# Performance work log

Hardware: AMD Instinct MI355X
Metric: run time of the kernel (lower is better)

The kernel has to match this reference:

```python
import jax, jax.numpy as jnp
import numpy as np

DIM = 768
HEADS = 12
HD = DIM // HEADS
E = 8
R = 64
ALPHA = 128.0
LORA_SCALE = ALPHA / R  # 2.0
ENABLE_BITS = np.array([1.0, 0.0, 1.0], dtype=np.float32)  # LoRA on q and v slices of qkv


def setup_inputs() -> dict:
    key = jax.random.key(0)
    ks = jax.random.split(key, 8)
    x = jax.random.normal(ks[0], (2, 4096, DIM), jnp.float32)
    # base (frozen) weights, shared across experts; no biases (qkv_bias=False)
    Wqkv = jax.random.normal(ks[1], (3 * DIM, DIM), jnp.float32) * 0.02
    Wproj = jax.random.normal(ks[2], (DIM, DIM), jnp.float32) * 0.02
    # per-expert LoRA adapters. qkv: shared down-proj A, per-output-slice up-proj B,
    # masked by enable bits (q,k,v).
    Aqkv = jax.random.normal(ks[3], (E, R, DIM), jnp.float32) * 0.02
    Bqkv = jax.random.normal(ks[4], (E, 3, DIM, R), jnp.float32) * 0.02
    Bqkv = Bqkv * jnp.asarray(ENABLE_BITS)[None, :, None, None]
    Aproj = jax.random.normal(ks[5], (E, R, DIM), jnp.float32) * 0.02
    Bproj = jax.random.normal(ks[6], (E, DIM, R), jnp.float32) * 0.02
    expert_indices = np.arange(4, dtype=np.int64) % E  # static per-chunk routing
    chunk_sizes = np.array([1024, 1024, 1024, 1024], dtype=np.int64)
    return {"x": x, "Wqkv": Wqkv, "Aqkv": Aqkv, "Bqkv": Bqkv, "Wproj": Wproj,
            "Aproj": Aproj, "Bproj": Bproj, "expert_indices": expert_indices,
            "chunk_sizes": chunk_sizes}


def reference(x, Wqkv, Aqkv, Bqkv, Wproj, Aproj, Bproj, expert_indices, chunk_sizes):
    # chunk sizes / expert indices are static host-side routing metadata
    sizes = [int(c) for c in np.asarray(chunk_sizes)]
    eidx = [int(e) for e in np.asarray(expert_indices)]
    offs = np.concatenate([[0], np.cumsum(sizes)])
    B = x.shape[0]
    scale = HD ** -0.5
    last_k = None
    last_v = None
    outs = []
    for i, n in enumerate(sizes):
        xc = x[:, offs[i]:offs[i + 1]]            # [B, n, DIM]
        e = eidx[i]
        # LoRA-adapted qkv for this chunk's expert
        base = xc @ Wqkv.T                        # [B, n, 3*DIM]
        h = xc @ Aqkv[e].T                        # [B, n, R]
        delta = jnp.einsum('bnr,tdr->bntd', h, Bqkv[e]).reshape(B, n, 3 * DIM)
        qkv = (base + LORA_SCALE * delta).reshape(B, n, 3, HEADS, HD)
        qkv = qkv.transpose(2, 0, 3, 1, 4)        # [3, B, H, n, HD]
        q, k, v = qkv[0], qkv[1], qkv[2]
        if last_k is not None:                    # growing KV over chunks (chunk-causal)
            k = jnp.concatenate([last_k, k], axis=-2)
            v = jnp.concatenate([last_v, v], axis=-2)
        last_k, last_v = k, v
        attn = jax.nn.softmax(jnp.einsum('bhqd,bhkd->bhqk', q * scale, k), axis=-1)
        o = jnp.einsum('bhqk,bhkd->bhqd', attn, v)
        o = o.transpose(0, 2, 1, 3).reshape(B, n, DIM)
        # LoRA-adapted output projection for the same expert
        o = o @ Wproj.T + LORA_SCALE * ((o @ Aproj[e].T) @ Bproj[e].T)
        outs.append(o)
    return jnp.concatenate(outs, axis=1)          # [B, total, DIM]
```

## Files before the change

kernel.cpp:

```cpp
#include <hip/hip_runtime.h>
#include <math.h>

#define BATCH   2
#define SEQ     4096
#define DIMD    768
#define NHEADS  12
#define HDIM    64
#define RR      64
#define CHUNK   1024
#define NTOK    (BATCH * SEQ)
#define BHN     (BATCH * NHEADS)
#define PITCH   88
#define KC2     2304
#define QSCALE  0.18033688011112042f

typedef __attribute__((ext_vector_type(8))) short short8;
typedef __attribute__((ext_vector_type(4))) float f32x4;

#define AS1 __attribute__((address_space(1)))
#define AS3 __attribute__((address_space(3)))

__device__ __forceinline__ void glds16(const void* g, void* l) {
    __builtin_amdgcn_global_load_lds((const AS1 unsigned int*)g,
                                     (AS3 unsigned int*)l, 16, 0, 0);
}

__device__ __forceinline__ float dot4(const float4 a, const float4 b) {
    float s = a.x * b.x;
    s = fmaf(a.y, b.y, s);
    s = fmaf(a.z, b.z, s);
    s = fmaf(a.w, b.w, s);
    return s;
}

__device__ __forceinline__ unsigned short f2bf(float x) {
    union { float f; unsigned u; } c; c.f = x;
    unsigned u = c.u + 0x7fffu + ((c.u >> 16) & 1u);
    return (unsigned short)(u >> 16);
}
__device__ __forceinline__ float bf2f(unsigned short h) {
    union { unsigned u; float f; } c; c.u = ((unsigned)h) << 16;
    return c.f;
}
__device__ __forceinline__ unsigned pack2bf(float a, float b) {
    union { float f; unsigned u; } x, y; x.f = a; y.f = b;
    unsigned ua = x.u + 0x7fffu + ((x.u >> 16) & 1u);
    unsigned ub = y.u + 0x7fffu + ((y.u >> 16) & 1u);
    return (ua >> 16) | (ub & 0xffff0000u);
}

__global__ __launch_bounds__(256)
void combine_split(const float* __restrict__ W, const float* __restrict__ A,
                   const float* __restrict__ Bm, int NB,
                   unsigned short* __restrict__ out)
{
    const int tid = threadIdx.x;
    const int ty = tid >> 4, tx = tid & 15;
    const int f0 = blockIdx.x * 64, d0 = blockIdx.y * 64, e = blockIdx.z;

    __shared__ float Bb[64][68];
    __shared__ float Aa[64][68];

    const float* Ae = A + (long)e * RR * DIMD;
    const float* Be = Bm + (long)e * NB * RR;

    const int lrow = tid >> 2, lc = (tid & 3) * 16;
    #pragma unroll
    for (int u = 0; u < 16; u += 4)
        *(float4*)&Bb[lrow][lc + u] = *(const float4*)&Be[(long)(f0 + lrow) * RR + lc + u];
    #pragma unroll
    for (int u = 0; u < 16; u++)
        Aa[lc + u][lrow] = Ae[(long)lrow * DIMD + d0 + lc + u];
    __syncthreads();

    float acc[4][4] = {};
    #pragma unroll
    for (int r4 = 0; r4 < RR; r4 += 4) {
        float4 a[4], b[4];
        #pragma unroll
        for (int i = 0; i < 4; i++) a[i] = *(float4*)&Bb[ty + 16 * i][r4];
        #pragma unroll
        for (int j = 0; j < 4; j++) b[j] = *(float4*)&Aa[tx + 16 * j][r4];
        #pragma unroll
        for (int i = 0; i < 4; i++)
            #pragma unroll
            for (int j = 0; j < 4; j++)
                acc[i][j] += dot4(a[i], b[j]);
    }

    #pragma unroll
    for (int i = 0; i < 4; i++) {
        const int f = f0 + ty + 16 * i;
        unsigned short* o = out + ((long)e * NB + f) * KC2;
        #pragma unroll
        for (int j = 0; j < 4; j++) {
            const int d = d0 + tx + 16 * j;
            const float val = W[(long)f * DIMD + d] + 2.0f * acc[i][j];
            const unsigned short hi = f2bf(val);
            const unsigned short lo = f2bf(val - bf2f(hi));
            o[d] = hi; o[768 + d] = lo; o[1536 + d] = hi;
        }
    }
}

__global__ __launch_bounds__(192)
void build_xa2(const float* __restrict__ X, unsigned short* __restrict__ out)
{
    const int tok = blockIdx.x;
    const int j = threadIdx.x * 4;
    const float* xr = X + (long)tok * DIMD;
    unsigned short* o = out + (long)tok * KC2;
    float4 v = *(const float4*)&xr[j];
    unsigned short h0 = f2bf(v.x), h1 = f2bf(v.y), h2 = f2bf(v.z), h3 = f2bf(v.w);
    unsigned short l0 = f2bf(v.x - bf2f(h0)), l1 = f2bf(v.y - bf2f(h1));
    unsigned short l2 = f2bf(v.z - bf2f(h2)), l3 = f2bf(v.w - bf2f(h3));
    uint2 hp, lp;
    hp.x = (unsigned)h0 | ((unsigned)h1 << 16);
    hp.y = (unsigned)h2 | ((unsigned)h3 << 16);
    lp.x = (unsigned)l0 | ((unsigned)l1 << 16);
    lp.y = (unsigned)l2 | ((unsigned)l3 << 16);
    *(uint2*)&o[j] = hp;
    *(uint2*)&o[768 + j] = hp;
    *(uint2*)&o[1536 + j] = lp;
}

template<int MODE>
__global__ __launch_bounds__(256)
void mfma_gemm(const unsigned short* __restrict__ A,
               const unsigned short* __restrict__ B, int NB, int n_base,
               unsigned short* __restrict__ qpl, unsigned short* __restrict__ kpl,
               unsigned short* __restrict__ vpl, float* __restrict__ outf)
{
    __shared__ __align__(16) unsigned short lA[128 * 64];
    __shared__ __align__(16) unsigned short lB[128 * 64];

    const int tid = threadIdx.x;
    const int lane = tid & 63;
    const int wave = tid >> 6;
    const int n = lane & 15;
    const int quad = lane >> 4;
    const int wm = wave & 1, wn = wave >> 1;

    const int m0 = blockIdx.x * 128;
    const int n0 = n_base + blockIdx.y * 128;
    const int e = (m0 & (SEQ - 1)) >> 10;
    const unsigned short* Ap = A + (long)m0 * KC2;
    const unsigned short* Bp = B + ((long)e * NB + n0) * KC2;

    long soff[4];
    int sldsoff = wave * 1024;
    #pragma unroll
    for (int iss = 0; iss < 4; iss++) {
        const int g = iss * 256 + tid;
        const int row = g >> 3;
        const int gc = (g & 7) ^ (row & 7);
        soff[iss] = (long)row * KC2 + gc * 8;
    }

    f32x4 acc[4][4];
    #pragma unroll
    for (int i = 0; i < 4; i++)
        #pragma unroll
        for (int j = 0; j < 4; j++)
            acc[i][j] = (f32x4){0.f, 0.f, 0.f, 0.f};

    for (int k0 = 0; k0 < KC2; k0 += 64) {
        __syncthreads();
        #pragma unroll
        for (int iss = 0; iss < 4; iss++) {
            glds16(Ap + soff[iss] + k0, (char*)lA + iss * 4096 + sldsoff);
            glds16(Bp + soff[iss] + k0, (char*)lB + iss * 4096 + sldsoff);
        }
        __builtin_amdgcn_s_waitcnt(0);
        __syncthreads();

        #pragma unroll
        for (int kk = 0; kk < 2; kk++) {
            const int kg = kk * 4;
            short8 af[4], bfr[4];
            #pragma unroll
            for (int mt = 0; mt < 4; mt++) {
                const int r = wm * 64 + mt * 16 + n;
                const int p = (kg + quad) ^ (r & 7);
                af[mt] = *(const short8*)&lA[r * 64 + p * 8];
            }
            #pragma unroll
            for (int nt = 0; nt < 4; nt++) {
                const int r = wn * 64 + nt * 16 + n;
                const int p = (kg + quad) ^ (r & 7);
                bfr[nt] = *(const short8*)&lB[r * 64 + p * 8];
            }
            #pragma unroll
            for (int mt = 0; mt < 4; mt++)
                #pragma unroll
                for (int nt = 0; nt < 4; nt++) {
                    if (MODE == 1)
                        acc[mt][nt] = __builtin_amdgcn_mfma_f32_16x16x32_bf16(
                            af[mt], bfr[nt], acc[mt][nt], 0, 0, 0);
                    else
                        acc[mt][nt] = __builtin_amdgcn_mfma_f32_16x16x32_bf16(
                            bfr[nt], af[mt], acc[mt][nt], 0, 0, 0);
                }
        }
    }

    #pragma unroll
    for (int mt = 0; mt < 4; mt++) {
        #pragma unroll
        for (int nt = 0; nt < 4; nt++) {
            f32x4 a = acc[mt][nt];
            if (MODE == 0) {
                const int fb = n0 + wn * 64 + nt * 16 + quad * 4;
                const int t = fb >= 768 ? 1 : 0;
                const int rem = fb - t * 768;
                const int head = rem >> 6;
                const int d0 = rem & 63;
                const int token = m0 + wm * 64 + mt * 16 + n;
                const int b = token >> 12, s = token & (SEQ - 1);
                const int bh = b * NHEADS + head;
                const float sc = t ? 1.0f : QSCALE;
                unsigned short* dst = (t ? kpl : qpl) + ((long)(bh * SEQ + s)) * HDIM + d0;
                uint2 pk;
                pk.x = pack2bf(a[0] * sc, a[1] * sc);
                pk.y = pack2bf(a[2] * sc, a[3] * sc);
                *(uint2*)dst = pk;
            } else if (MODE == 1) {
                const int f = n0 + wn * 64 + nt * 16 + n;
                const int head = (f - 1536) >> 6;
                const int d = f & 63;
                const int tok0 = m0 + wm * 64 + mt * 16 + quad * 4;
                const int b = tok0 >> 12, s0 = tok0 & (SEQ - 1);
                const int bh = b * NHEADS + head;
                unsigned short* dst = vpl + ((long)(bh * HDIM + d)) * SEQ + s0;
                uint2 pk;
                pk.x = pack2bf(a[0], a[1]);
                pk.y = pack2bf(a[2], a[3]);
                *(uint2*)dst = pk;
            } else {
                const int fb = n0 + wn * 64 + nt * 16 + quad * 4;
                const int token = m0 + wm * 64 + mt * 16 + n;
                *(f32x4*)&outf[(long)token * DIMD + fb] = a;
            }
        }
    }
}

__global__ __launch_bounds__(256)
void attn_mfma(const unsigned short* __restrict__ qp,
               const unsigned short* __restrict__ kpl,
               const unsigned short* __restrict__ vtp,
               float* __restrict__ ob)
{
    __shared__ unsigned short lK[64 * PITCH];
    __shared__ unsigned short lV[64 * PITCH];
    __shared__ __align__(16) unsigned short lP[4][32 * 64];

    const int tid = threadIdx.x;
    const int lane = tid & 63;
    const int wave = tid >> 6;
    const int n = lane & 15;
    const int quad = lane >> 4;

    const int qb = blockIdx.x;
    const int bh = blockIdx.y;
    const int ci = 3 - (int)blockIdx.z;
    const int b = bh / NHEADS;
    const int h = bh - b * NHEADS;

    const long planeQK = (long)bh * SEQ * HDIM;
    const long planeVt = (long)bh * HDIM * SEQ;
    const int q0 = ci * CHUNK + qb * 128 + wave * 32;
    const int nk = (ci + 1) * CHUNK;

    short8 qf[2][2];
    #pragma unroll
    for (int qt = 0; qt < 2; qt++)
        #pragma unroll
        for (int s = 0; s < 2; s++)
            qf[qt][s] = *(const short8*)&qp[planeQK + (long)(q0 + qt * 16 + n) * HDIM + s * 32 + quad * 8];

    f32x4 acc[4][2];
    #pragma unroll
    for (int m2 = 0; m2 < 4; m2++)
        #pragma unroll
        for (int qt = 0; qt < 2; qt++)
            acc[m2][qt] = (f32x4){0.f, 0.f, 0.f, 0.f};
    float lpart[2] = {0.f, 0.f};

    unsigned short* Pw = &lP[wave][0];
    const int c7 = n & 7;

    for (int k0 = 0; k0 < nk; k0 += 64) {
        __syncthreads();
        #pragma unroll
        for (int p = 0; p < 2; p++) {
            const int g = tid + p * 256;
            const int row = g >> 3, c8 = (g & 7) * 8;
            short8 kv = *(const short8*)&kpl[planeQK + (long)(k0 + row) * HDIM + c8];
            short8 vv = *(const short8*)&vtp[planeVt + (long)row * SEQ + k0 + c8];
            *(short8*)&lK[row * PITCH + c8] = kv;
            *(short8*)&lV[row * PITCH + c8] = vv;
        }
        __syncthreads();

        f32x4 st[4][2];
        #pragma unroll
        for (int kt = 0; kt < 4; kt++) {
            st[kt][0] = (f32x4){0.f, 0.f, 0.f, 0.f};
            st[kt][1] = (f32x4){0.f, 0.f, 0.f, 0.f};
        }
        #pragma unroll
        for (int s = 0; s < 2; s++) {
            #pragma unroll
            for (int kt = 0; kt < 4; kt++) {
                short8 kf = *(const short8*)&lK[(kt * 16 + n) * PITCH + s * 32 + quad * 8];
                st[kt][0] = __builtin_amdgcn_mfma_f32_16x16x32_bf16(kf, qf[0][s], st[kt][0], 0, 0, 0);
                st[kt][1] = __builtin_amdgcn_mfma_f32_16x16x32_bf16(kf, qf[1][s], st[kt][1], 0, 0, 0);
            }
        }

        #pragma unroll
        for (int qt = 0; qt < 2; qt++) {
            unsigned short* prow = Pw + (qt * 16 + n) * 64;
            #pragma unroll
            for (int kt = 0; kt < 4; kt++) {
                const float e0 = __builtin_exp2f(st[kt][qt][0]);
                const float e1 = __builtin_exp2f(st[kt][qt][1]);
                const float e2 = __builtin_exp2f(st[kt][qt][2]);
                const float e3 = __builtin_exp2f(st[kt][qt][3]);
                lpart[qt] += (e0 + e1) + (e2 + e3);
                uint2 pkv;
                pkv.x = pack2bf(e0, e1);
                pkv.y = pack2bf(e2, e3);
                const int gsw = (2 * kt + (quad >> 1)) ^ c7;
                *(uint2*)&prow[gsw * 8 + (quad & 1) * 4] = pkv;
            }
        }

        #pragma unroll
        for (int hh = 0; hh < 2; hh++) {
            short8 pf[2];
            #pragma unroll
            for (int qt = 0; qt < 2; qt++) {
                const int gsw = (hh * 4 + quad) ^ c7;
                pf[qt] = *(const short8*)&Pw[(qt * 16 + n) * 64 + gsw * 8];
            }
            #pragma unroll
            for (int m2 = 0; m2 < 4; m2++) {
                short8 vf = *(const short8*)&lV[(m2 * 16 + n) * PITCH + hh * 32 + quad * 8];
                acc[m2][0] = __builtin_amdgcn_mfma_f32_16x16x32_bf16(vf, pf[0], acc[m2][0], 0, 0, 0);
                acc[m2][1] = __builtin_amdgcn_mfma_f32_16x16x32_bf16(vf, pf[1], acc[m2][1], 0, 0, 0);
            }
        }
    }

    #pragma unroll
    for (int qt = 0; qt < 2; qt++) {
        lpart[qt] += __shfl_xor(lpart[qt], 16, 64);
        lpart[qt] += __shfl_xor(lpart[qt], 32, 64);
    }

    #pragma unroll
    for (int qt = 0; qt < 2; qt++) {
        const float inv = 1.0f / lpart[qt];
        const int token = b * SEQ + q0 + qt * 16 + n;
        #pragma unroll
        for (int m2 = 0; m2 < 4; m2++) {
            f32x4 r = acc[m2][qt] * inv;
            *(f32x4*)&ob[(long)token * DIMD + h * HDIM + m2 * 16 + quad * 4] = r;
        }
    }
}

extern "C" void kernel_launch(void* const* d_in, const int* in_sizes, int n_in,
                              void* d_out, int out_size, void* d_ws, size_t ws_size,
                              hipStream_t stream) {
    (void)in_sizes; (void)n_in; (void)out_size; (void)ws_size;
    const float* x     = (const float*)d_in[0];
    const float* Wqkv  = (const float*)d_in[1];
    const float* Aqkv  = (const float*)d_in[2];
    const float* Bqkv  = (const float*)d_in[3];
    const float* Wproj = (const float*)d_in[4];
    const float* Aproj = (const float*)d_in[5];
    const float* Bproj = (const float*)d_in[6];

    char* wsb = (char*)d_ws;
    unsigned short* XA   = (unsigned short*)(wsb);
    unsigned short* WBq  = (unsigned short*)(wsb + (38l << 20));
    float*          o_buf = (float*)(wsb + (38l << 20));
    unsigned short* WBp  = (unsigned short*)(wsb + (80l << 20));
    unsigned short* qpl  = (unsigned short*)(wsb + (94l << 20));
    unsigned short* kpl  = (unsigned short*)(wsb + (107l << 20));
    unsigned short* vpl  = (unsigned short*)(wsb + (120l << 20));

    dim3 blk(256);

    combine_split<<<dim3(36, 12, 4), blk, 0, stream>>>(Wqkv, Aqkv, Bqkv, 3 * DIMD, WBq);
    combine_split<<<dim3(12, 12, 4), blk, 0, stream>>>(Wproj, Aproj, Bproj, DIMD, WBp);
    build_xa2<<<dim3(NTOK), dim3(192), 0, stream>>>(x, XA);
    mfma_gemm<0><<<dim3(NTOK / 128, 12), blk, 0, stream>>>(XA, WBq, 3 * DIMD, 0,    qpl, kpl, vpl, nullptr);
    mfma_gemm<1><<<dim3(NTOK / 128, 6),  blk, 0, stream>>>(XA, WBq, 3 * DIMD, 1536, qpl, kpl, vpl, nullptr);
    attn_mfma<<<dim3(8, BHN, 4), blk, 0, stream>>>(qpl, kpl, vpl, o_buf);
    build_xa2<<<dim3(NTOK), dim3(192), 0, stream>>>(o_buf, XA);
    mfma_gemm<2><<<dim3(NTOK / 128, 6), blk, 0, stream>>>(XA, WBp, DIMD, 0, nullptr, nullptr, nullptr, (float*)d_out);
}
```

Baseline: 457.0 us.

## Fuse attention epilogue into bf16 split XA, use direct-to-LDS loads and MFMA row sums

The attention kernel now writes its output directly as the hi/hi/lo bf16-split activation layout the projection GEMM consumes, removing the fp32 o_buf round trip and a build_xa2 launch. K/V tiles are loaded with global_load_lds into XOR-swizzled unpadded LDS instead of register-staged padded copies. The softmax denominator is accumulated via an extra MFMA against a ones vector rather than scalar adds and shuffles. P packing uses perm-based bf16 rounding. This adds a waitcnt(0) before the barrier and relies on the swizzle being consistent between writer and reader.

```diff
diff --git a/kernel.cpp b/kernel.cpp
--- a/kernel.cpp
+++ b/kernel.cpp
@@ -10,7 +10,6 @@
 #define CHUNK   1024
 #define NTOK    (BATCH * SEQ)
 #define BHN     (BATCH * NHEADS)
-#define PITCH   88
 #define KC2     2304
 #define QSCALE  0.18033688011112042f
 
@@ -249,10 +248,10 @@
 void attn_mfma(const unsigned short* __restrict__ qp,
                const unsigned short* __restrict__ kpl,
                const unsigned short* __restrict__ vtp,
-               float* __restrict__ ob)
+               unsigned short* __restrict__ XA)
 {
-    __shared__ unsigned short lK[64 * PITCH];
-    __shared__ unsigned short lV[64 * PITCH];
+    __shared__ __align__(16) unsigned short lK[64 * 64];
+    __shared__ __align__(16) unsigned short lV[64 * 64];
     __shared__ __align__(16) unsigned short lP[4][32 * 64];
 
     const int tid = threadIdx.x;
@@ -260,6 +259,7 @@
     const int wave = tid >> 6;
     const int n = lane & 15;
     const int quad = lane >> 4;
+    const int c7 = n & 7;
 
     const int qb = blockIdx.x;
     const int bh = blockIdx.y;
@@ -272,6 +272,16 @@
     const int q0 = ci * CHUNK + qb * 128 + wave * 32;
     const int nk = (ci + 1) * CHUNK;
 
+    long skoff[2], svoff[2];
+    #pragma unroll
+    for (int p = 0; p < 2; p++) {
+        const int g = (wave * 2 + p) * 64 + lane;
+        const int row = g >> 3;
+        const int gc = (g & 7) ^ (row & 7);
+        skoff[p] = (long)row * HDIM + gc * 8;
+        svoff[p] = (long)row * SEQ + gc * 8;
+    }
+
     short8 qf[2][2];
     #pragma unroll
     for (int qt = 0; qt < 2; qt++)
@@ -279,28 +289,27 @@
         for (int s = 0; s < 2; s++)
             qf[qt][s] = *(const short8*)&qp[planeQK + (long)(q0 + qt * 16 + n) * HDIM + s * 32 + quad * 8];
 
+    const short8 ones8 = {0x3f80, 0x3f80, 0x3f80, 0x3f80, 0x3f80, 0x3f80, 0x3f80, 0x3f80};
+
     f32x4 acc[4][2];
+    f32x4 accl[2];
     #pragma unroll
     for (int m2 = 0; m2 < 4; m2++)
         #pragma unroll
         for (int qt = 0; qt < 2; qt++)
             acc[m2][qt] = (f32x4){0.f, 0.f, 0.f, 0.f};
-    float lpart[2] = {0.f, 0.f};
+    accl[0] = (f32x4){0.f, 0.f, 0.f, 0.f};
+    accl[1] = (f32x4){0.f, 0.f, 0.f, 0.f};
 
     unsigned short* Pw = &lP[wave][0];
-    const int c7 = n & 7;
 
     for (int k0 = 0; k0 < nk; k0 += 64) {
         __syncthreads();
-        #pragma unroll
-        for (int p = 0; p < 2; p++) {
-            const int g = tid + p * 256;
-            const int row = g >> 3, c8 = (g & 7) * 8;
-            short8 kv = *(const short8*)&kpl[planeQK + (long)(k0 + row) * HDIM + c8];
-            short8 vv = *(const short8*)&vtp[planeVt + (long)row * SEQ + k0 + c8];
-            *(short8*)&lK[row * PITCH + c8] = kv;
-            *(short8*)&lV[row * PITCH + c8] = vv;
-        }
+        glds16(kpl + planeQK + (long)k0 * HDIM + skoff[0], (char*)lK + wave * 2048);
+        glds16(kpl + planeQK + (long)k0 * HDIM + skoff[1], (char*)lK + wave * 2048 + 1024);
+        glds16(vtp + planeVt + k0 + svoff[0], (char*)lV + wave * 2048);
+        glds16(vtp + planeVt + k0 + svoff[1], (char*)lV + wave * 2048 + 1024);
+        __builtin_amdgcn_s_waitcnt(0);
         __syncthreads();
 
         f32x4 st[4][2];
@@ -313,7 +322,8 @@
         for (int s = 0; s < 2; s++) {
             #pragma unroll
             for (int kt = 0; kt < 4; kt++) {
-                short8 kf = *(const short8*)&lK[(kt * 16 + n) * PITCH + s * 32 + quad * 8];
+                const int gr = (s * 4 + quad) ^ c7;
+                short8 kf = *(const short8*)&lK[(kt * 16 + n) * 64 + gr * 8];
                 st[kt][0] = __builtin_amdgcn_mfma_f32_16x16x32_bf16(kf, qf[0][s], st[kt][0], 0, 0, 0);
                 st[kt][1] = __builtin_amdgcn_mfma_f32_16x16x32_bf16(kf, qf[1][s], st[kt][1], 0, 0, 0);
             }
@@ -324,14 +334,13 @@
             unsigned short* prow = Pw + (qt * 16 + n) * 64;
             #pragma unroll
             for (int kt = 0; kt < 4; kt++) {
-                const float e0 = __builtin_exp2f(st[kt][qt][0]);
-                const float e1 = __builtin_exp2f(st[kt][qt][1]);
-                const float e2 = __builtin_exp2f(st[kt][qt][2]);
-                const float e3 = __builtin_exp2f(st[kt][qt][3]);
-                lpart[qt] += (e0 + e1) + (e2 + e3);
+                const unsigned u0 = __float_as_uint(__builtin_exp2f(st[kt][qt][0])) + 0x8000u;
+                const unsigned u1 = __float_as_uint(__builtin_exp2f(st[kt][qt][1])) + 0x8000u;
+                const unsigned u2 = __float_as_uint(__builtin_exp2f(st[kt][qt][2])) + 0x8000u;
+                const unsigned u3 = __float_as_uint(__builtin_exp2f(st[kt][qt][3])) + 0x8000u;
                 uint2 pkv;
-                pkv.x = pack2bf(e0, e1);
-                pkv.y = pack2bf(e2, e3);
+                pkv.x = __builtin_amdgcn_perm(u1, u0, 0x07060302);
+                pkv.y = __builtin_amdgcn_perm(u3, u2, 0x07060302);
                 const int gsw = (2 * kt + (quad >> 1)) ^ c7;
                 *(uint2*)&prow[gsw * 8 + (quad & 1) * 4] = pkv;
             }
@@ -347,27 +356,38 @@
             }
             #pragma unroll
             for (int m2 = 0; m2 < 4; m2++) {
-                short8 vf = *(const short8*)&lV[(m2 * 16 + n) * PITCH + hh * 32 + quad * 8];
+                const int gr = (hh * 4 + quad) ^ c7;
+                short8 vf = *(const short8*)&lV[(m2 * 16 + n) * 64 + gr * 8];
                 acc[m2][0] = __builtin_amdgcn_mfma_f32_16x16x32_bf16(vf, pf[0], acc[m2][0], 0, 0, 0);
                 acc[m2][1] = __builtin_amdgcn_mfma_f32_16x16x32_bf16(vf, pf[1], acc[m2][1], 0, 0, 0);
             }
+            accl[0] = __builtin_amdgcn_mfma_f32_16x16x32_bf16(ones8, pf[0], accl[0], 0, 0, 0);
+            accl[1] = __builtin_amdgcn_mfma_f32_16x16x32_bf16(ones8, pf[1], accl[1], 0, 0, 0);
         }
     }
 
     #pragma unroll
     for (int qt = 0; qt < 2; qt++) {
-        lpart[qt] += __shfl_xor(lpart[qt], 16, 64);
-        lpart[qt] += __shfl_xor(lpart[qt], 32, 64);
-    }
-
-    #pragma unroll
-    for (int qt = 0; qt < 2; qt++) {
-        const float inv = 1.0f / lpart[qt];
+        const float inv = 1.0f / accl[qt][0];
         const int token = b * SEQ + q0 + qt * 16 + n;
+        unsigned short* xrow = XA + (long)token * KC2;
         #pragma unroll
         for (int m2 = 0; m2 < 4; m2++) {
-            f32x4 r = acc[m2][qt] * inv;
-            *(f32x4*)&ob[(long)token * DIMD + h * HDIM + m2 * 16 + quad * 4] = r;
+            const int d = h * HDIM + m2 * 16 + quad * 4;
+            const float o0 = acc[m2][qt][0] * inv;
+            const float o1 = acc[m2][qt][1] * inv;
+            const float o2 = acc[m2][qt][2] * inv;
+            const float o3 = acc[m2][qt][3] * inv;
+            const unsigned short h0 = f2bf(o0), h1 = f2bf(o1);
+            const unsigned short h2 = f2bf(o2), h3 = f2bf(o3);
+            uint2 hp, lp;
+            hp.x = (unsigned)h0 | ((unsigned)h1 << 16);
+            hp.y = (unsigned)h2 | ((unsigned)h3 << 16);
+            lp.x = pack2bf(o0 - bf2f(h0), o1 - bf2f(h1));
+            lp.y = pack2bf(o2 - bf2f(h2), o3 - bf2f(h3));
+            *(uint2*)&xrow[d] = hp;
+            *(uint2*)&xrow[768 + d] = hp;
+            *(uint2*)&xrow[1536 + d] = lp;
         }
     }
 }
@@ -387,7 +407,6 @@
     char* wsb = (char*)d_ws;
     unsigned short* XA   = (unsigned short*)(wsb);
     unsigned short* WBq  = (unsigned short*)(wsb + (38l << 20));
-    float*          o_buf = (float*)(wsb + (38l << 20));
     unsigned short* WBp  = (unsigned short*)(wsb + (80l << 20));
     unsigned short* qpl  = (unsigned short*)(wsb + (94l << 20));
     unsigned short* kpl  = (unsigned short*)(wsb + (107l << 20));
@@ -400,7 +419,6 @@
     build_xa2<<<dim3(NTOK), dim3(192), 0, stream>>>(x, XA);
     mfma_gemm<0><<<dim3(NTOK / 128, 12), blk, 0, stream>>>(XA, WBq, 3 * DIMD, 0,    qpl, kpl, vpl, nullptr);
     mfma_gemm<1><<<dim3(NTOK / 128, 6),  blk, 0, stream>>>(XA, WBq, 3 * DIMD, 1536, qpl, kpl, vpl, nullptr);
-    attn_mfma<<<dim3(8, BHN, 4), blk, 0, stream>>>(qpl, kpl, vpl, o_buf);
-    build_xa2<<<dim3(NTOK), dim3(192), 0, stream>>>(o_buf, XA);
+    attn_mfma<<<dim3(8, BHN, 4), blk, 0, stream>>>(qpl, kpl, vpl, XA);
     mfma_gemm<2><<<dim3(NTOK / 128, 6), blk, 0, stream>>>(XA, WBp, DIMD, 0, nullptr, nullptr, nullptr, (float*)d_out);
 }
```

Measured after the change: 441.1 us. 3.5% less time.
